# Optimization experiments

Hardware: AMD Instinct MI355X
Metric: run time of the kernel (lower is better)

## Reference

```python
import jax, jax.numpy as jnp
import numpy as np

N_ATOMS = 8192
N_PAIRS = 65536
F = 128        # n_atombasis
R = 20         # n_radialbasis
B = 5          # graph_n_blocks
EPS = 1e-8     # stability constant


def setup_inputs() -> dict:
    key = jax.random.key(0)
    ks = jax.random.split(key, 16)
    rn = lambda k, shape, s=0.05: jax.random.normal(k, shape, dtype=jnp.float32) * s
    return {
        "features": jax.random.normal(ks[0], (N_ATOMS, F), jnp.float32),
        "distances": jax.random.uniform(ks[1], (N_PAIRS,), jnp.float32, 0.5, 5.0),
        "vectors": jax.random.normal(ks[2], (N_PAIRS, 3), jnp.float32),
        "cutoffs": jax.random.uniform(ks[3], (N_PAIRS,), jnp.float32),
        "rbfs": jax.random.normal(ks[4], (N_PAIRS, R), jnp.float32),
        "filter_W": rn(ks[5], (R, B * 3 * F)),
        "filter_b": jnp.zeros((B * 3 * F,), jnp.float32),
        "int_W1": rn(ks[6], (B, F, F)),
        "int_b1": jnp.zeros((B, F), jnp.float32),
        "int_W2": rn(ks[7], (B, F, 3 * F)),
        "int_b2": jnp.zeros((B, 3 * F), jnp.float32),
        "mix_Wv": rn(ks[8], (B, F, 2 * F)),
        "mix_W1": rn(ks[9], (B, 2 * F, F)),
        "mix_b1": jnp.zeros((B, F), jnp.float32),
        "mix_W2": rn(ks[10], (B, F, 3 * F)),
        "mix_b2": jnp.zeros((B, 3 * F), jnp.float32),
        "idx_i": jax.random.randint(ks[11], (N_PAIRS,), 0, N_ATOMS),
        "idx_j": jax.random.randint(ks[12], (N_PAIRS,), 0, N_ATOMS),
    }


def reference(features, distances, vectors, cutoffs, rbfs,
              filter_W, filter_b, int_W1, int_b1, int_W2, int_b2,
              mix_Wv, mix_W1, mix_b1, mix_W2, mix_b2, idx_i, idx_j):
    n_atoms = features.shape[0]
    # Cutoff-weighted radial filters, one (3F) chunk per block: [P, B*3F]
    descriptors = (rbfs @ filter_W + filter_b) * cutoffs[:, None]
    dir_ij = vectors / distances[:, None]                       # [P, 3]

    q = features[:, None, :]                                    # [N, 1, F]
    mu = jnp.zeros((n_atoms, 3, F), dtype=features.dtype)       # [N, 3, F]

    for b in range(B):
        # --- interaction block ---
        x = jax.nn.silu(q @ int_W1[b] + int_b1[b]) @ int_W2[b] + int_b2[b]  # [N,1,3F]
        Wij = descriptors[:, None, b * 3 * F:(b + 1) * 3 * F]               # [P,1,3F]
        xj = x[idx_j] * Wij                                                 # [P,1,3F]
        muj = mu[idx_j]                                                     # [P,3,F]
        dq, dmuR, dmumu = jnp.split(xj, 3, axis=-1)                         # [P,1,F] each
        dmu = dmuR * dir_ij[:, :, None] + dmumu * muj                       # [P,3,F]
        q = q + jax.ops.segment_sum(dq, idx_i, num_segments=n_atoms)
        mu = mu + jax.ops.segment_sum(dmu, idx_i, num_segments=n_atoms)

        # --- mixing block ---
        mu_V, mu_W = jnp.split(mu @ mix_Wv[b], 2, axis=-1)                  # [N,3,F] each
        mu_Vn = jnp.sqrt(jnp.sum(mu_V ** 2, axis=-2, keepdims=True) + EPS)  # [N,1,F]
        ctx = jnp.concatenate([q, mu_Vn], axis=-1)                          # [N,1,2F]
        y = jax.nn.silu(ctx @ mix_W1[b] + mix_b1[b]) @ mix_W2[b] + mix_b2[b]
        dq_i, dmu_i, dqmu_i = jnp.split(y, 3, axis=-1)                      # [N,1,F] each
        q = q + dq_i + dqmu_i * jnp.sum(mu_V * mu_W, axis=1, keepdims=True)
        mu = mu + dmu_i * mu_W

    return q[:, 0, :], mu
```

## Files before the change

### kernel.cpp

```cpp
#include <hip/hip_runtime.h>
#include <hip/hip_bf16.h>

#define NA 8192
#define NP 65536
#define WROW 1920
#define CAP 40
#define PLANE 1048576

typedef short short8 __attribute__((ext_vector_type(8)));
typedef short short4v __attribute__((ext_vector_type(4)));
typedef float floatx4 __attribute__((ext_vector_type(4)));

static __device__ __forceinline__ short f2bf(float f) {
    union { float f; unsigned u; } v; v.f = f;
    unsigned r = v.u + 0x7FFF + ((v.u >> 16) & 1);
    return (short)(r >> 16);
}
static __device__ __forceinline__ float bf2f(short s) {
    union { unsigned u; float f; } v;
    v.u = ((unsigned)(unsigned short)s) << 16;
    return v.f;
}
static __device__ __forceinline__ unsigned char f2fp8(float f) {
    int p = __builtin_amdgcn_cvt_pk_fp8_f32(f, 0.f, 0, false);
    return (unsigned char)(p & 0xFF);
}
static __device__ __forceinline__ float fp82f(unsigned char b) {
    return __builtin_amdgcn_cvt_f32_fp8((int)b, 0);
}
static __device__ __forceinline__ float silu(float v) {
    return v / (1.f + __expf(-v));
}

static __device__ __forceinline__ void swz(const float* __restrict__ src,
                                           short* __restrict__ dst,
                                           int K, int N, int idx) {
    int kn = K * N;
    int b = idx / kn;
    int r = idx - b * kn;
    int tile = r >> 9, li = r & 511;
    int lane = li >> 3, bb = li & 7;
    int Kt = K >> 5;
    int nt = tile / Kt, kt = tile - nt * Kt;
    int k = kt * 32 + (lane >> 4) * 8 + bb;
    int n = nt * 16 + (lane & 15);
    dst[idx] = f2bf(src[b * kn + k * N + n]);
}

__global__ __launch_bounds__(256) void k_setup(const float* __restrict__ iW1,
                                               const float* __restrict__ iW2,
                                               const float* __restrict__ mWv,
                                               const float* __restrict__ mW1,
                                               const float* __restrict__ mW2,
                                               const float* __restrict__ fW,
                                               short* __restrict__ W1t,
                                               short* __restrict__ W2t,
                                               short* __restrict__ Wvt,
                                               short* __restrict__ mW1t,
                                               short* __restrict__ mW2t,
                                               short* __restrict__ fWt,
                                               const float* __restrict__ feat,
                                               float* __restrict__ q,
                                               float* __restrict__ mu,
                                               short* __restrict__ q_bf,
                                               unsigned short* __restrict__ mp0,
                                               int* __restrict__ cursor) {
    int idx = blockIdx.x * 256 + threadIdx.x;
    if (idx < 962560) {
        if (idx < 81920)       { swz(iW1, W1t, 128, 128, idx); return; }
        idx -= 81920;
        if (idx < 245760)      { swz(iW2, W2t, 128, 384, idx); return; }
        idx -= 245760;
        if (idx < 163840)      { swz(mWv, Wvt, 128, 256, idx); return; }
        idx -= 163840;
        if (idx < 163840)      { swz(mW1, mW1t, 256, 128, idx); return; }
        idx -= 163840;
        if (idx < 245760)      { swz(mW2, mW2t, 128, 384, idx); return; }
        idx -= 245760;
        {
            int b = idx / 12288;
            int r = idx - b * 12288;
            int nt = r >> 9;
            int li = r & 511;
            int lane = li >> 3, bb = li & 7;
            int k = (lane >> 4) * 8 + bb;
            int n = nt * 16 + (lane & 15);
            fWt[b * 12288 + r] = (k < 20) ? f2bf(fW[k * WROW + b * 384 + n]) : (short)0;
        }
        return;
    }
    idx -= 962560;
    if (idx < NA * 128) { float v = feat[idx]; q[idx] = v; q_bf[idx] = f2bf(v); }
    mu[idx] = 0.f;
    mp0[idx] = 0;
    if (idx < NA) cursor[idx] = 0;
}

__global__ __launch_bounds__(256) void k_fillprep(const int* __restrict__ idx_i,
                                                  const int* __restrict__ idx_j,
                                                  int* __restrict__ cursor,
                                                  const float* __restrict__ cut,
                                                  const float* __restrict__ dist,
                                                  const float* __restrict__ vec,
                                                  const float* __restrict__ rbfs,
                                                  float* __restrict__ cut_csr,
                                                  float4* __restrict__ dirj,
                                                  short* __restrict__ rbf_c) {
    int p = blockIdx.x * 256 + threadIdx.x;
    if (p >= NP) return;
    int i = idx_i[p];
    int pos = atomicAdd(&cursor[i], 1);
    if (pos >= CAP) return;
    int e = i * CAP + pos;
    float c = cut[p];
    cut_csr[e] = c;
    float invd = 1.f / dist[p];
    float4 d;
    d.x = vec[p * 3 + 0] * invd;
    d.y = vec[p * 3 + 1] * invd;
    d.z = vec[p * 3 + 2] * invd;
    d.w = __int_as_float(idx_j[p]);
    dirj[e] = d;
    #pragma unroll
    for (int k = 0; k < 20; ++k) rbf_c[e * 32 + k] = f2bf(rbfs[p * 20 + k] * c);
    #pragma unroll
    for (int k = 20; k < 32; ++k) rbf_c[e * 32 + k] = 0;
}

__global__ __launch_bounds__(256) void k_x(const short* __restrict__ q_bf,
                                           const short* __restrict__ W1sw,
                                           const short* __restrict__ W2sw,
                                           const float* __restrict__ b1,
                                           const float* __restrict__ b2,
                                           unsigned char* __restrict__ xp) {
    __shared__ __align__(16) short qtile[16 * 136];
    __shared__ __align__(16) short hs[16 * 136];
    int t = threadIdx.x;
    int wv = t >> 6, lane = t & 63, quad = lane >> 4, l16 = lane & 15;
    int a0 = blockIdx.x * 16;

    #pragma unroll
    for (int it = 0; it < 2; ++it) {
        int c = it * 256 + t;
        int row = c >> 5, col4 = c & 31;
        *(short4v*)(qtile + row * 136 + col4 * 4) =
            *(const short4v*)(q_bf + (a0 + row) * 128 + col4 * 4);
    }
    __syncthreads();

    floatx4 acc0 = {0.f, 0.f, 0.f, 0.f}, acc1 = {0.f, 0.f, 0.f, 0.f};
    #pragma unroll
    for (int kk = 0; kk < 4; ++kk) {
        short8 a  = *(const short8*)(qtile + l16 * 136 + kk * 32 + quad * 8);
        short8 b0 = *(const short8*)(W1sw + ((wv * 2 + 0) * 4 + kk) * 512 + lane * 8);
        short8 bq = *(const short8*)(W1sw + ((wv * 2 + 1) * 4 + kk) * 512 + lane * 8);
        acc0 = __builtin_amdgcn_mfma_f32_16x16x32_bf16(a, b0, acc0, 0, 0, 0);
        acc1 = __builtin_amdgcn_mfma_f32_16x16x32_bf16(a, bq, acc1, 0, 0, 0);
    }
    __syncthreads();
    {
        int n0 = wv * 32 + l16;
        float bia0 = b1[n0], bia1 = b1[n0 + 16];
        #pragma unroll
        for (int r = 0; r < 4; ++r) {
            int m = quad * 4 + r;
            hs[m * 136 + n0]      = f2bf(silu(acc0[r] + bia0));
            hs[m * 136 + n0 + 16] = f2bf(silu(acc1[r] + bia1));
        }
    }
    __syncthreads();
    floatx4 acc[6];
    #pragma unroll
    for (int jj = 0; jj < 6; ++jj) acc[jj] = {0.f, 0.f, 0.f, 0.f};
    #pragma unroll
    for (int kk = 0; kk < 4; ++kk) {
        short8 a = *(const short8*)(hs + l16 * 136 + kk * 32 + quad * 8);
        #pragma unroll
        for (int jj = 0; jj < 6; ++jj) {
            short8 b = *(const short8*)(W2sw + ((wv * 6 + jj) * 4 + kk) * 512 + lane * 8);
            acc[jj] = __builtin_amdgcn_mfma_f32_16x16x32_bf16(a, b, acc[jj], 0, 0, 0);
        }
    }
    #pragma unroll
    for (int jj = 0; jj < 6; ++jj) {
        int n = wv * 96 + jj * 16 + l16;
        float bia = b2[n];
        #pragma unroll
        for (int r = 0; r < 4; ++r) {
            int m = quad * 4 + r;
            xp[(size_t)(n >> 7) * PLANE + (size_t)(a0 + m) * 128 + (n & 127)] =
                f2fp8(acc[jj][r] + bia);
        }
    }
}

__global__ __launch_bounds__(256, 4) void k_gather(const unsigned char* __restrict__ xp_r,
                                                   const unsigned short* __restrict__ mp_r,
                                                   const short* __restrict__ rbf_c,
                                                   const short* __restrict__ fWt,
                                                   const float* __restrict__ fbp,
                                                   const float4* __restrict__ dirj,
                                                   const float* __restrict__ cut_csr,
                                                   const int* __restrict__ cursor,
                                                   short* __restrict__ dqg,
                                                   short* __restrict__ dmug) {
    __shared__ short dlds[16 * 392];
    __shared__ float pm[3 * 512];
    int i = blockIdx.x;
    int t = threadIdx.x;
    int wv = t >> 6, lane = t & 63, quad = lane >> 4, l16 = lane & 15;
    int start = i * CAP;
    int f0 = lane * 2;

    float4 dj[4];
    #pragma unroll
    for (int m = 0; m < 4; ++m) dj[m] = dirj[start + wv + 4 * m];
    short8 afrag = *(const short8*)(rbf_c + (size_t)(start + l16) * 32 + quad * 8);
    float cc[4];
    #pragma unroll
    for (int r = 0; r < 4; ++r) cc[r] = cut_csr[start + quad * 4 + r];

    int cnt = cursor[i];
    if (cnt > CAP) cnt = CAP;
    int end = start + cnt;

    float acc[8];
    #pragma unroll
    for (int k = 0; k < 8; ++k) acc[k] = 0.f;

    for (int e0 = start; e0 < end; e0 += 16) {
        if (e0 > start) {
            __syncthreads();
            #pragma unroll
            for (int m = 0; m < 4; ++m) dj[m] = dirj[e0 + wv + 4 * m];
            afrag = *(const short8*)(rbf_c + (size_t)(e0 + l16) * 32 + quad * 8);
            #pragma unroll
            for (int r = 0; r < 4; ++r) cc[r] = cut_csr[e0 + quad * 4 + r];
        }
        int clen = end - e0; if (clen > 16) clen = 16;
        #pragma unroll
        for (int nt = 0; nt < 6; ++nt) {
            int col = wv * 96 + nt * 16 + l16;
            short8 bfr = *(const short8*)(fWt + (wv * 6 + nt) * 512 + lane * 8);
            floatx4 z = {0.f, 0.f, 0.f, 0.f};
            floatx4 ad = __builtin_amdgcn_mfma_f32_16x16x32_bf16(afrag, bfr, z, 0, 0, 0);
            float fbv = fbp[col];
            dlds[(quad * 4 + 0) * 392 + col] = f2bf(ad[0] + fbv * cc[0]);
            dlds[(quad * 4 + 1) * 392 + col] = f2bf(ad[1] + fbv * cc[1]);
            dlds[(quad * 4 + 2) * 392 + col] = f2bf(ad[2] + fbv * cc[2]);
            dlds[(quad * 4 + 3) * 392 + col] = f2bf(ad[3] + fbv * cc[3]);
        }
        unsigned short xr0[4], xr1[4], xr2[4];
        unsigned mr0[4], mr1[4], mr2[4];
        #pragma unroll
        for (int m = 0; m < 4; ++m) {
            int le = wv + 4 * m;
            int j = (le < clen) ? __float_as_int(dj[m].w) : 0;
            size_t bx = (size_t)j * 128 + f0;
            xr0[m] = *(const unsigned short*)(xp_r + bx);
            xr1[m] = *(const unsigned short*)(xp_r + PLANE + bx);
            xr2[m] = *(const unsigned short*)(xp_r + 2 * PLANE + bx);
            mr0[m] = *(const unsigned*)(mp_r + bx);
            mr1[m] = *(const unsigned*)(mp_r + PLANE + bx);
            mr2[m] = *(const unsigned*)(mp_r + 2 * PLANE + bx);
        }
        __syncthreads();
        #pragma unroll
        for (int m = 0; m < 4; ++m) {
            int le = wv + 4 * m;
            if (le < clen) {
                unsigned wa = *(const unsigned*)(dlds + le * 392 + f0);
                unsigned wb = *(const unsigned*)(dlds + le * 392 + 128 + f0);
                unsigned wc = *(const unsigned*)(dlds + le * 392 + 256 + f0);
                float wa0 = bf2f((short)(wa & 0xFFFF)), wa1 = bf2f((short)(wa >> 16));
                float wb0 = bf2f((short)(wb & 0xFFFF)), wb1 = bf2f((short)(wb >> 16));
                float wc0 = bf2f((short)(wc & 0xFFFF)), wc1 = bf2f((short)(wc >> 16));
                {
                    float x0 = fp82f((unsigned char)(xr0[m] & 0xFF));
                    float x1 = fp82f((unsigned char)(xr1[m] & 0xFF));
                    float x2 = fp82f((unsigned char)(xr2[m] & 0xFF));
                    float u0 = bf2f((short)(mr0[m] & 0xFFFF));
                    float u1 = bf2f((short)(mr1[m] & 0xFFFF));
                    float u2 = bf2f((short)(mr2[m] & 0xFFFF));
                    acc[0] += x0 * wa0;
                    float xb = x1 * wb0, xc = x2 * wc0;
                    acc[1] += xb * dj[m].x + xc * u0;
                    acc[2] += xb * dj[m].y + xc * u1;
                    acc[3] += xb * dj[m].z + xc * u2;
                }
                {
                    float x0 = fp82f((unsigned char)(xr0[m] >> 8));
                    float x1 = fp82f((unsigned char)(xr1[m] >> 8));
                    float x2 = fp82f((unsigned char)(xr2[m] >> 8));
                    float u0 = bf2f((short)(mr0[m] >> 16));
                    float u1 = bf2f((short)(mr1[m] >> 16));
                    float u2 = bf2f((short)(mr2[m] >> 16));
                    acc[4] += x0 * wa1;
                    float xb = x1 * wb1, xc = x2 * wc1;
                    acc[5] += xb * dj[m].x + xc * u0;
                    acc[6] += xb * dj[m].y + xc * u1;
                    acc[7] += xb * dj[m].z + xc * u2;
                }
            }
        }
    }
    if (wv) {
        float* p = pm + (wv - 1) * 512;
        #pragma unroll
        for (int arr = 0; arr < 4; ++arr) {
            float2 v; v.x = acc[arr]; v.y = acc[arr + 4];
            *(float2*)(p + arr * 128 + f0) = v;
        }
    }
    __syncthreads();
    if (wv == 0) {
        #pragma unroll
        for (int arr = 0; arr < 4; ++arr) {
            float2 p0 = *(const float2*)(pm + 0 * 512 + arr * 128 + f0);
            float2 p1 = *(const float2*)(pm + 1 * 512 + arr * 128 + f0);
            float2 p2 = *(const float2*)(pm + 2 * 512 + arr * 128 + f0);
            float sl = acc[arr]     + p0.x + p1.x + p2.x;
            float sh = acc[arr + 4] + p0.y + p1.y + p2.y;
            unsigned o = (unsigned)(unsigned short)f2bf(sl) |
                         ((unsigned)(unsigned short)f2bf(sh) << 16);
            if (arr == 0) *(unsigned*)(dqg + i * 128 + f0) = o;
            else          *(unsigned*)(dmug + (i * 3 + arr - 1) * 128 + f0) = o;
        }
    }
}

__global__ __launch_bounds__(512, 4) void k_mixx(const float* __restrict__ mu_ro,
                                                 const short* __restrict__ dmug,
                                                 const float* __restrict__ q_ro,
                                                 const short* __restrict__ dqg,
                                                 const short* __restrict__ Wvsw,
                                                 const short* __restrict__ W1sw,
                                                 const short* __restrict__ W2sw,
                                                 const float* __restrict__ b1,
                                                 const float* __restrict__ b2,
                                                 float* __restrict__ q,
                                                 float* __restrict__ mu,
                                                 unsigned char* __restrict__ xp_w,
                                                 unsigned short* __restrict__ mp_w,
                                                 const short* __restrict__ xW1sw,
                                                 const short* __restrict__ xW2sw,
                                                 const float* __restrict__ xb1,
                                                 const float* __restrict__ xb2,
                                                 int do_x) {
    __shared__ __align__(16) char smem[51968];
    short* ms    = (short*)(smem);
    short* qtile = (short*)(smem + 13056);
    short* Vv    = (short*)(smem + 17408);
    short* hs    = (short*)(smem + 17408);
    short* Vw    = (short*)(smem + 30464);
    short* vnb   = (short*)(smem + 43520);
    short* sb    = (short*)(smem + 47872);
    unsigned char* xls = (unsigned char*)(smem + 43520);
    int t = threadIdx.x;
    int wv = t >> 6, lane = t & 63, quad = lane >> 4, l16 = lane & 15;
    int a0 = blockIdx.x * 16;
    int co = wv * 16 + l16;

    float qnf[4];
    float mnf[4][3];
    #pragma unroll
    for (int r = 0; r < 4; ++r) {
        int m = quad * 4 + r;
        int ga = a0 + m;
        int gq = ga * 128 + co;
        qnf[r] = q_ro[gq] + bf2f(dqg[gq]);
        qtile[m * 136 + co] = f2bf(qnf[r]);
        #pragma unroll
        for (int d = 0; d < 3; ++d) {
            int gm = (ga * 3 + d) * 128 + co;
            mnf[r][d] = mu_ro[gm] + bf2f(dmug[gm]);
            ms[(m * 3 + d) * 136 + co] = f2bf(mnf[r][d]);
        }
    }
    __syncthreads();

    {
        floatx4 acc[3][2];
        #pragma unroll
        for (int mt = 0; mt < 3; ++mt)
            #pragma unroll
            for (int nt = 0; nt < 2; ++nt) acc[mt][nt] = {0.f, 0.f, 0.f, 0.f};
        #pragma unroll
        for (int kk = 0; kk < 4; ++kk) {
            short8 a[3];
            #pragma unroll
            for (int mt = 0; mt < 3; ++mt)
                a[mt] = *(const short8*)(ms + (mt * 16 + l16) * 136 + kk * 32 + quad * 8);
            #pragma unroll
            for (int nt = 0; nt < 2; ++nt) {
                short8 b = *(const short8*)(Wvsw + ((wv * 2 + nt) * 4 + kk) * 512 + lane * 8);
                #pragma unroll
                for (int mt = 0; mt < 3; ++mt)
                    acc[mt][nt] = __builtin_amdgcn_mfma_f32_16x16x32_bf16(a[mt], b, acc[mt][nt], 0, 0, 0);
            }
        }
        #pragma unroll
        for (int mt = 0; mt < 3; ++mt)
            #pragma unroll
            for (int nt = 0; nt < 2; ++nt)
                #pragma unroll
                for (int r = 0; r < 4; ++r) {
                    int row = mt * 16 + quad * 4 + r;
                    int col = wv * 32 + nt * 16 + l16;
                    short v = f2bf(acc[mt][nt][r]);
                    if (col < 128) Vv[row * 136 + col] = v;
                    else           Vw[row * 136 + col - 128] = v;
                }
    }
    __syncthreads();
    #pragma unroll
    for (int k = 0; k < 4; ++k) {
        int idx = k * 512 + t;
        int a = idx >> 7, c = idx & 127;
        float v0 = bf2f(Vv[(a * 3 + 0) * 136 + c]);
        float v1 = bf2f(Vv[(a * 3 + 1) * 136 + c]);
        float v2 = bf2f(Vv[(a * 3 + 2) * 136 + c]);
        float w0 = bf2f(Vw[(a * 3 + 0) * 136 + c]);
        float w1 = bf2f(Vw[(a * 3 + 1) * 136 + c]);
        float w2 = bf2f(Vw[(a * 3 + 2) * 136 + c]);
        vnb[a * 136 + c] = f2bf(sqrtf(v0 * v0 + v1 * v1 + v2 * v2 + 1e-8f));
        sb[a * 128 + c]  = f2bf(v0 * w0 + v1 * w1 + v2 * w2);
    }
    __syncthreads();
    {
        floatx4 accq = {0.f, 0.f, 0.f, 0.f};
        floatx4 accv = {0.f, 0.f, 0.f, 0.f};
        #pragma unroll
        for (int kk = 0; kk < 4; ++kk) {
            short8 aq = *(const short8*)(qtile + l16 * 136 + kk * 32 + quad * 8);
            short8 av = *(const short8*)(vnb + l16 * 136 + kk * 32 + quad * 8);
            short8 bq = *(const short8*)(W1sw + (wv * 8 + kk) * 512 + lane * 8);
            short8 bv = *(const short8*)(W1sw + (wv * 8 + 4 + kk) * 512 + lane * 8);
            accq = __builtin_amdgcn_mfma_f32_16x16x32_bf16(aq, bq, accq, 0, 0, 0);
            accv = __builtin_amdgcn_mfma_f32_16x16x32_bf16(av, bv, accv, 0, 0, 0);
        }
        int n0 = wv * 16 + l16;
        float bia0 = b1[n0];
        #pragma unroll
        for (int r = 0; r < 4; ++r) {
            int m = quad * 4 + r;
            hs[m * 136 + n0] = f2bf(silu(accq[r] + accv[r] + bia0));
        }
    }
    __syncthreads();
    {
        floatx4 accB[3];
        #pragma unroll
        for (int c = 0; c < 3; ++c) accB[c] = {0.f, 0.f, 0.f, 0.f};
        #pragma unroll
        for (int kk = 0; kk < 4; ++kk) {
            short8 a = *(const short8*)(hs + l16 * 136 + kk * 32 + quad * 8);
            #pragma unroll
            for (int c = 0; c < 3; ++c) {
                short8 b = *(const short8*)(W2sw + ((c * 8 + wv) * 4 + kk) * 512 + lane * 8);
                accB[c] = __builtin_amdgcn_mfma_f32_16x16x32_bf16(a, b, accB[c], 0, 0, 0);
            }
        }
        float bq_  = b2[co];
        float bm_  = b2[128 + co];
        float bqm_ = b2[256 + co];
        #pragma unroll
        for (int r = 0; r < 4; ++r) {
            int m = quad * 4 + r;
            int ga = a0 + m;
            float dq   = accB[0][r] + bq_;
            float dmu  = accB[1][r] + bm_;
            float dqmu = accB[2][r] + bqm_;
            float sv = bf2f(sb[m * 128 + co]);
            int gq = ga * 128 + co;
            float qn = qnf[r] + dq + dqmu * sv;
            q[gq] = qn;
            qtile[m * 136 + co] = f2bf(qn);
            float mn[3];
            #pragma unroll
            for (int d = 0; d < 3; ++d) {
                int gm = (ga * 3 + d) * 128 + co;
                float mw = bf2f(Vw[(m * 3 + d) * 136 + co]);
                mn[d] = mnf[r][d] + dmu * mw;
                mu[gm] = mn[d];
            }
            if (do_x) {
                mp_w[(size_t)0 * PLANE + gq] = (unsigned short)f2bf(mn[0]);
                mp_w[(size_t)1 * PLANE + gq] = (unsigned short)f2bf(mn[1]);
                mp_w[(size_t)2 * PLANE + gq] = (unsigned short)f2bf(mn[2]);
            }
        }
    }
    if (!do_x) return;
    __syncthreads();
    {
        floatx4 acc0 = {0.f, 0.f, 0.f, 0.f};
        #pragma unroll
        for (int kk = 0; kk < 4; ++kk) {
            short8 a  = *(const short8*)(qtile + l16 * 136 + kk * 32 + quad * 8);
            short8 b0 = *(const short8*)(xW1sw + (wv * 4 + kk) * 512 + lane * 8);
            acc0 = __builtin_amdgcn_mfma_f32_16x16x32_bf16(a, b0, acc0, 0, 0, 0);
        }
        int n0 = wv * 16 + l16;
        float bia0 = xb1[n0];
        #pragma unroll
        for (int r = 0; r < 4; ++r) {
            int m = quad * 4 + r;
            hs[m * 136 + n0] = f2bf(silu(acc0[r] + bia0));
        }
    }
    __syncthreads();
    {
        floatx4 acc[3];
        #pragma unroll
        for (int jj = 0; jj < 3; ++jj) acc[jj] = {0.f, 0.f, 0.f, 0.f};
        #pragma unroll
        for (int kk = 0; kk < 4; ++kk) {
            short8 a = *(const short8*)(hs + l16 * 136 + kk * 32 + quad * 8);
            #pragma unroll
            for (int jj = 0; jj < 3; ++jj) {
                short8 b = *(const short8*)(xW2sw + ((wv * 3 + jj) * 4 + kk) * 512 + lane * 8);
                acc[jj] = __builtin_amdgcn_mfma_f32_16x16x32_bf16(a, b, acc[jj], 0, 0, 0);
            }
        }
        #pragma unroll
        for (int jj = 0; jj < 3; ++jj) {
            int n = wv * 48 + jj * 16 + l16;
            float bia = xb2[n];
            #pragma unroll
            for (int r = 0; r < 4; ++r) {
                int m = quad * 4 + r;
                xls[(n >> 7) * 2048 + m * 128 + (n & 127)] = f2fp8(acc[jj][r] + bia);
            }
        }
    }
    __syncthreads();
    {
        const unsigned* xlsu = (const unsigned*)xls;
        #pragma unroll
        for (int k = 0; k < 3; ++k) {
            int idx = k * 512 + t;
            int p = idx >> 9;
            int wo = idx & 511;
            *(unsigned*)(xp_w + (size_t)p * PLANE + (size_t)a0 * 128 + wo * 4) = xlsu[idx];
        }
    }
}

extern "C" void kernel_launch(void* const* d_in, const int* in_sizes, int n_in,
                              void* d_out, int out_size, void* d_ws, size_t ws_size,
                              hipStream_t stream) {
    const float* feat = (const float*)d_in[0];
    const float* dist = (const float*)d_in[1];
    const float* vec  = (const float*)d_in[2];
    const float* cut  = (const float*)d_in[3];
    const float* rbfs = (const float*)d_in[4];
    const float* fW   = (const float*)d_in[5];
    const float* fb   = (const float*)d_in[6];
    const float* iW1  = (const float*)d_in[7];
    const float* ib1  = (const float*)d_in[8];
    const float* iW2  = (const float*)d_in[9];
    const float* ib2  = (const float*)d_in[10];
    const float* mWv  = (const float*)d_in[11];
    const float* mW1  = (const float*)d_in[12];
    const float* mb1  = (const float*)d_in[13];
    const float* mW2  = (const float*)d_in[14];
    const float* mb2  = (const float*)d_in[15];
    const int* idx_i  = (const int*)d_in[16];
    const int* idx_j  = (const int*)d_in[17];

    float* q  = (float*)d_out;
    float* mu = (float*)d_out + NA * 128;

    char* w = (char*)d_ws;
    unsigned char*  xp0 = (unsigned char*)(w);
    unsigned char*  xp1 = (unsigned char*)(w + 3145728);
    unsigned short* mp0 = (unsigned short*)(w + 6291456);
    unsigned short* mp1 = (unsigned short*)(w + 12582912);
    short* dqg     = (short*)(w + 18874368);
    short* dmug    = (short*)(w + 20971520);
    short* q_bf    = (short*)(w + 27262976);
    short* W1t     = (short*)(w + 29360128);
    short* W2t     = (short*)(w + 29523968);
    short* Wvt     = (short*)(w + 30015488);
    short* mW1t    = (short*)(w + 30343168);
    short* mW2t    = (short*)(w + 30670848);
    short* fWt     = (short*)(w + 31162368);
    int*   cursor  = (int*)(w + 31285248);
    float4* dirj   = (float4*)(w + 31318016);
    float* cut_csr = (float*)(w + 36561152);
    short* rbf_c   = (short*)(w + 37871936);

    k_setup<<<16048, 256, 0, stream>>>(iW1, iW2, mWv, mW1, mW2, fW,
                                       W1t, W2t, Wvt, mW1t, mW2t, fWt,
                                       feat, q, mu, q_bf, mp0, cursor);
    k_fillprep<<<NP / 256, 256, 0, stream>>>(idx_i, idx_j, cursor, cut, dist, vec,
                                             rbfs, cut_csr, dirj, rbf_c);

    k_x<<<NA / 16, 256, 0, stream>>>(q_bf, W1t, W2t, ib1, ib2, xp0);
    unsigned char*  xa[2] = {xp0, xp1};
    unsigned short* ma[2] = {mp0, mp1};
    for (int b = 0; b < 5; ++b) {
        int bn = (b + 1) % 5;
        k_gather<<<NA, 256, 0, stream>>>(xa[b & 1], ma[b & 1], rbf_c, fWt + b * 12288,
                                         fb + b * 384, dirj, cut_csr, cursor,
                                         dqg, dmug);
        k_mixx<<<NA / 16, 512, 0, stream>>>(mu, dmug, q, dqg,
                                            Wvt + b * 32768,
                                            mW1t + b * 32768, mW2t + b * 49152,
                                            mb1 + b * 128, mb2 + b * 384,
                                            q, mu,
                                            xa[(b + 1) & 1], ma[(b + 1) & 1],
                                            W1t + bn * 16384, W2t + bn * 49152,
                                            ib1 + bn * 128, ib2 + bn * 384,
                                            (b < 4) ? 1 : 0);
    }
}
```

Measured before the change: 356.3 us.

## Process four atoms per gather block with prefetch of next atom's edge data

Each k_gather block now handles four consecutive atoms instead of one, so the grid shrinks by a factor of four. The per-edge direction, rbf fragment and cutoff values for the next atom are loaded during the last chunk of the current atom so their latency overlaps compute. This cuts block launch and setup overhead, but each block runs serially over its atoms with extra barriers and uses more registers. That can reduce occupancy and leave fewer blocks to hide gather latency.

```diff
diff --git a/kernel.cpp b/kernel.cpp
--- a/kernel.cpp
+++ b/kernel.cpp
@@ -206,125 +206,159 @@
                                                    short* __restrict__ dmug) {
     __shared__ short dlds[16 * 392];
     __shared__ float pm[3 * 512];
-    int i = blockIdx.x;
     int t = threadIdx.x;
     int wv = t >> 6, lane = t & 63, quad = lane >> 4, l16 = lane & 15;
-    int start = i * CAP;
     int f0 = lane * 2;
-
-    float4 dj[4];
-    #pragma unroll
-    for (int m = 0; m < 4; ++m) dj[m] = dirj[start + wv + 4 * m];
-    short8 afrag = *(const short8*)(rbf_c + (size_t)(start + l16) * 32 + quad * 8);
-    float cc[4];
-    #pragma unroll
-    for (int r = 0; r < 4; ++r) cc[r] = cut_csr[start + quad * 4 + r];
-
-    int cnt = cursor[i];
-    if (cnt > CAP) cnt = CAP;
-    int end = start + cnt;
-
-    float acc[8];
-    #pragma unroll
-    for (int k = 0; k < 8; ++k) acc[k] = 0.f;
-
-    for (int e0 = start; e0 < end; e0 += 16) {
-        if (e0 > start) {
+    int base = blockIdx.x * 4;
+    int4 cnt4 = *(const int4*)(cursor + base);
+
+    float4 dj[4]; short8 afrag; float cc[4];
+    {
+        int s0 = base * CAP;
+        #pragma unroll
+        for (int m = 0; m < 4; ++m) dj[m] = dirj[s0 + wv + 4 * m];
+        afrag = *(const short8*)(rbf_c + (size_t)(s0 + l16) * 32 + quad * 8);
+        #pragma unroll
+        for (int r = 0; r < 4; ++r) cc[r] = cut_csr[s0 + quad * 4 + r];
+    }
+    float4 djP[4]; short8 afP; float ccP[4]; int pfv = 0;
+
+    for (int ai = 0; ai < 4; ++ai) {
+        int i = base + ai;
+        int start = i * CAP;
+        int cnt = (ai == 0) ? cnt4.x : (ai == 1) ? cnt4.y : (ai == 2) ? cnt4.z : cnt4.w;
+        if (cnt > CAP) cnt = CAP;
+        int end = start + cnt;
+
+        if (ai > 0) {
+            if (pfv) {
+                #pragma unroll
+                for (int m = 0; m < 4; ++m) dj[m] = djP[m];
+                afrag = afP;
+                #pragma unroll
+                for (int r = 0; r < 4; ++r) cc[r] = ccP[r];
+            } else {
+                #pragma unroll
+                for (int m = 0; m < 4; ++m) dj[m] = dirj[start + wv + 4 * m];
+                afrag = *(const short8*)(rbf_c + (size_t)(start + l16) * 32 + quad * 8);
+                #pragma unroll
+                for (int r = 0; r < 4; ++r) cc[r] = cut_csr[start + quad * 4 + r];
+            }
+            pfv = 0;
+        }
+
+        float acc[8];
+        #pragma unroll
+        for (int k = 0; k < 8; ++k) acc[k] = 0.f;
+
+        for (int e0 = start; e0 < end; e0 += 16) {
+            if (e0 > start) {
+                __syncthreads();
+                #pragma unroll
+                for (int m = 0; m < 4; ++m) dj[m] = dirj[e0 + wv + 4 * m];
+                afrag = *(const short8*)(rbf_c + (size_t)(e0 + l16) * 32 + quad * 8);
+                #pragma unroll
+                for (int r = 0; r < 4; ++r) cc[r] = cut_csr[e0 + quad * 4 + r];
+            }
+            int clen = end - e0; if (clen > 16) clen = 16;
+            #pragma unroll
+            for (int nt = 0; nt < 6; ++nt) {
+                int col = wv * 96 + nt * 16 + l16;
+                short8 bfr = *(const short8*)(fWt + (wv * 6 + nt) * 512 + lane * 8);
+                floatx4 z = {0.f, 0.f, 0.f, 0.f};
+                floatx4 ad = __builtin_amdgcn_mfma_f32_16x16x32_bf16(afrag, bfr, z, 0, 0, 0);
+                float fbv = fbp[col];
+                dlds[(quad * 4 + 0) * 392 + col] = f2bf(ad[0] + fbv * cc[0]);
+                dlds[(quad * 4 + 1) * 392 + col] = f2bf(ad[1] + fbv * cc[1]);
+                dlds[(quad * 4 + 2) * 392 + col] = f2bf(ad[2] + fbv * cc[2]);
+                dlds[(quad * 4 + 3) * 392 + col] = f2bf(ad[3] + fbv * cc[3]);
+            }
+            unsigned short xr0[4], xr1[4], xr2[4];
+            unsigned mr0[4], mr1[4], mr2[4];
+            #pragma unroll
+            for (int m = 0; m < 4; ++m) {
+                int le = wv + 4 * m;
+                int j = (le < clen) ? __float_as_int(dj[m].w) : 0;
+                size_t bx = (size_t)j * 128 + f0;
+                xr0[m] = *(const unsigned short*)(xp_r + bx);
+                xr1[m] = *(const unsigned short*)(xp_r + PLANE + bx);
+                xr2[m] = *(const unsigned short*)(xp_r + 2 * PLANE + bx);
+                mr0[m] = *(const unsigned*)(mp_r + bx);
+                mr1[m] = *(const unsigned*)(mp_r + PLANE + bx);
+                mr2[m] = *(const unsigned*)(mp_r + 2 * PLANE + bx);
+            }
+            if (ai < 3 && e0 + 16 >= end && !pfv) {
+                int s2 = (i + 1) * CAP;
+                #pragma unroll
+                for (int m = 0; m < 4; ++m) djP[m] = dirj[s2 + wv + 4 * m];
+                afP = *(const short8*)(rbf_c + (size_t)(s2 + l16) * 32 + quad * 8);
+                #pragma unroll
+                for (int r = 0; r < 4; ++r) ccP[r] = cut_csr[s2 + quad * 4 + r];
+                pfv = 1;
+            }
             __syncthreads();
             #pragma unroll
-            for (int m = 0; m < 4; ++m) dj[m] = dirj[e0 + wv + 4 * m];
-            afrag = *(const short8*)(rbf_c + (size_t)(e0 + l16) * 32 + quad * 8);
-            #pragma unroll
-            for (int r = 0; r < 4; ++r) cc[r] = cut_csr[e0 + quad * 4 + r];
-        }
-        int clen = end - e0; if (clen > 16) clen = 16;
-        #pragma unroll
-        for (int nt = 0; nt < 6; ++nt) {
-            int col = wv * 96 + nt * 16 + l16;
-            short8 bfr = *(const short8*)(fWt + (wv * 6 + nt) * 512 + lane * 8);
-            floatx4 z = {0.f, 0.f, 0.f, 0.f};
-            floatx4 ad = __builtin_amdgcn_mfma_f32_16x16x32_bf16(afrag, bfr, z, 0, 0, 0);
-            float fbv = fbp[col];
-            dlds[(quad * 4 + 0) * 392 + col] = f2bf(ad[0] + fbv * cc[0]);
-            dlds[(quad * 4 + 1) * 392 + col] = f2bf(ad[1] + fbv * cc[1]);
-            dlds[(quad * 4 + 2) * 392 + col] = f2bf(ad[2] + fbv * cc[2]);
-            dlds[(quad * 4 + 3) * 392 + col] = f2bf(ad[3] + fbv * cc[3]);
-        }
-        unsigned short xr0[4], xr1[4], xr2[4];
-        unsigned mr0[4], mr1[4], mr2[4];
-        #pragma unroll
-        for (int m = 0; m < 4; ++m) {
-            int le = wv + 4 * m;
-            int j = (le < clen) ? __float_as_int(dj[m].w) : 0;
-            size_t bx = (size_t)j * 128 + f0;
-            xr0[m] = *(const unsigned short*)(xp_r + bx);
-            xr1[m] = *(const unsigned short*)(xp_r + PLANE + bx);
-            xr2[m] = *(const unsigned short*)(xp_r + 2 * PLANE + bx);
-            mr0[m] = *(const unsigned*)(mp_r + bx);
-            mr1[m] = *(const unsigned*)(mp_r + PLANE + bx);
-            mr2[m] = *(const unsigned*)(mp_r + 2 * PLANE + bx);
+            for (int m = 0; m < 4; ++m) {
+                int le = wv + 4 * m;
+                if (le < clen) {
+                    unsigned wa = *(const unsigned*)(dlds + le * 392 + f0);
+                    unsigned wb = *(const unsigned*)(dlds + le * 392 + 128 + f0);
+                    unsigned wc = *(const unsigned*)(dlds + le * 392 + 256 + f0);
+                    float wa0 = bf2f((short)(wa & 0xFFFF)), wa1 = bf2f((short)(wa >> 16));
+                    float wb0 = bf2f((short)(wb & 0xFFFF)), wb1 = bf2f((short)(wb >> 16));
+                    float wc0 = bf2f((short)(wc & 0xFFFF)), wc1 = bf2f((short)(wc >> 16));
+                    {
+                        float x0 = fp82f((unsigned char)(xr0[m] & 0xFF));
+                        float x1 = fp82f((unsigned char)(xr1[m] & 0xFF));
+                        float x2 = fp82f((unsigned char)(xr2[m] & 0xFF));
+                        float u0 = bf2f((short)(mr0[m] & 0xFFFF));
+                        float u1 = bf2f((short)(mr1[m] & 0xFFFF));
+                        float u2 = bf2f((short)(mr2[m] & 0xFFFF));
+                        acc[0] += x0 * wa0;
+                        float xb = x1 * wb0, xc = x2 * wc0;
+                        acc[1] += xb * dj[m].x + xc * u0;
+                        acc[2] += xb * dj[m].y + xc * u1;
+                        acc[3] += xb * dj[m].z + xc * u2;
+                    }
+                    {
+                        float x0 = fp82f((unsigned char)(xr0[m] >> 8));
+                        float x1 = fp82f((unsigned char)(xr1[m] >> 8));
+                        float x2 = fp82f((unsigned char)(xr2[m] >> 8));
+                        float u0 = bf2f((short)(mr0[m] >> 16));
+                        float u1 = bf2f((short)(mr1[m] >> 16));
+                        float u2 = bf2f((short)(mr2[m] >> 16));
+                        acc[4] += x0 * wa1;
+                        float xb = x1 * wb1, xc = x2 * wc1;
+                        acc[5] += xb * dj[m].x + xc * u0;
+                        acc[6] += xb * dj[m].y + xc * u1;
+                        acc[7] += xb * dj[m].z + xc * u2;
+                    }
+                }
+            }
         }
         __syncthreads();
-        #pragma unroll
-        for (int m = 0; m < 4; ++m) {
-            int le = wv + 4 * m;
-            if (le < clen) {
-                unsigned wa = *(const unsigned*)(dlds + le * 392 + f0);
-                unsigned wb = *(const unsigned*)(dlds + le * 392 + 128 + f0);
-                unsigned wc = *(const unsigned*)(dlds + le * 392 + 256 + f0);
-                float wa0 = bf2f((short)(wa & 0xFFFF)), wa1 = bf2f((short)(wa >> 16));
-                float wb0 = bf2f((short)(wb & 0xFFFF)), wb1 = bf2f((short)(wb >> 16));
-                float wc0 = bf2f((short)(wc & 0xFFFF)), wc1 = bf2f((short)(wc >> 16));
-                {
-                    float x0 = fp82f((unsigned char)(xr0[m] & 0xFF));
-                    float x1 = fp82f((unsigned char)(xr1[m] & 0xFF));
-                    float x2 = fp82f((unsigned char)(xr2[m] & 0xFF));
-                    float u0 = bf2f((short)(mr0[m] & 0xFFFF));
-                    float u1 = bf2f((short)(mr1[m] & 0xFFFF));
-                    float u2 = bf2f((short)(mr2[m] & 0xFFFF));
-                    acc[0] += x0 * wa0;
-                    float xb = x1 * wb0, xc = x2 * wc0;
-                    acc[1] += xb * dj[m].x + xc * u0;
-                    acc[2] += xb * dj[m].y + xc * u1;
-                    acc[3] += xb * dj[m].z + xc * u2;
-                }
-                {
-                    float x0 = fp82f((unsigned char)(xr0[m] >> 8));
-                    float x1 = fp82f((unsigned char)(xr1[m] >> 8));
-                    float x2 = fp82f((unsigned char)(xr2[m] >> 8));
-                    float u0 = bf2f((short)(mr0[m] >> 16));
-                    float u1 = bf2f((short)(mr1[m] >> 16));
-                    float u2 = bf2f((short)(mr2[m] >> 16));
-                    acc[4] += x0 * wa1;
-                    float xb = x1 * wb1, xc = x2 * wc1;
-                    acc[5] += xb * dj[m].x + xc * u0;
-                    acc[6] += xb * dj[m].y + xc * u1;
-                    acc[7] += xb * dj[m].z + xc * u2;
-                }
-            }
-        }
-    }
-    if (wv) {
-        float* p = pm + (wv - 1) * 512;
-        #pragma unroll
-        for (int arr = 0; arr < 4; ++arr) {
-            float2 v; v.x = acc[arr]; v.y = acc[arr + 4];
-            *(float2*)(p + arr * 128 + f0) = v;
-        }
-    }
-    __syncthreads();
-    if (wv == 0) {
-        #pragma unroll
-        for (int arr = 0; arr < 4; ++arr) {
-            float2 p0 = *(const float2*)(pm + 0 * 512 + arr * 128 + f0);
-            float2 p1 = *(const float2*)(pm + 1 * 512 + arr * 128 + f0);
-            float2 p2 = *(const float2*)(pm + 2 * 512 + arr * 128 + f0);
-            float sl = acc[arr]     + p0.x + p1.x + p2.x;
-            float sh = acc[arr + 4] + p0.y + p1.y + p2.y;
-            unsigned o = (unsigned)(unsigned short)f2bf(sl) |
-                         ((unsigned)(unsigned short)f2bf(sh) << 16);
-            if (arr == 0) *(unsigned*)(dqg + i * 128 + f0) = o;
-            else          *(unsigned*)(dmug + (i * 3 + arr - 1) * 128 + f0) = o;
+        if (wv) {
+            float* p = pm + (wv - 1) * 512;
+            #pragma unroll
+            for (int arr = 0; arr < 4; ++arr) {
+                float2 v; v.x = acc[arr]; v.y = acc[arr + 4];
+                *(float2*)(p + arr * 128 + f0) = v;
+            }
+        }
+        __syncthreads();
+        if (wv == 0) {
+            #pragma unroll
+            for (int arr = 0; arr < 4; ++arr) {
+                float2 p0 = *(const float2*)(pm + 0 * 512 + arr * 128 + f0);
+                float2 p1 = *(const float2*)(pm + 1 * 512 + arr * 128 + f0);
+                float2 p2 = *(const float2*)(pm + 2 * 512 + arr * 128 + f0);
+                float sl = acc[arr]     + p0.x + p1.x + p2.x;
+                float sh = acc[arr + 4] + p0.y + p1.y + p2.y;
+                unsigned o = (unsigned)(unsigned short)f2bf(sl) |
+                             ((unsigned)(unsigned short)f2bf(sh) << 16);
+                if (arr == 0) *(unsigned*)(dqg + i * 128 + f0) = o;
+                else          *(unsigned*)(dmug + (i * 3 + arr - 1) * 128 + f0) = o;
+            }
         }
     }
 }
@@ -602,9 +636,9 @@
     unsigned short* ma[2] = {mp0, mp1};
     for (int b = 0; b < 5; ++b) {
         int bn = (b + 1) % 5;
-        k_gather<<<NA, 256, 0, stream>>>(xa[b & 1], ma[b & 1], rbf_c, fWt + b * 12288,
-                                         fb + b * 384, dirj, cut_csr, cursor,
-                                         dqg, dmug);
+        k_gather<<<NA / 4, 256, 0, stream>>>(xa[b & 1], ma[b & 1], rbf_c, fWt + b * 12288,
+                                             fb + b * 384, dirj, cut_csr, cursor,
+                                             dqg, dmug);
         k_mixx<<<NA / 16, 512, 0, stream>>>(mu, dmug, q, dqg,
                                             Wvt + b * 32768,
                                             mW1t + b * 32768, mW2t + b * 49152,
```

Result: slower. 564.8 us (+58.5%).

## Assign one wavefront per atom in gather kernel, removing block syncs and reduction

Applied to the files above, without the earlier changes.

The gather kernel now maps each wavefront to its own destination atom (four atoms per block) rather than spreading one atom's edges across four waves. Each wave computes its own descriptor tile with 24 MFMAs over 8-edge chunks, keeps it in a private LDS slice, and accumulates directly, which removes the __syncthreads barriers and the cross-wave LDS reduction. The cost is that each wave does the full descriptor MFMA work, with half of the 16-row MFMA output discarded because only 8 edges are used per chunk, and the per-wave gather loads run more serially with less latency hiding.

```diff
diff --git a/kernel.cpp b/kernel.cpp
--- a/kernel.cpp
+++ b/kernel.cpp
@@ -204,22 +204,14 @@
                                                    const int* __restrict__ cursor,
                                                    short* __restrict__ dqg,
                                                    short* __restrict__ dmug) {
-    __shared__ short dlds[16 * 392];
-    __shared__ float pm[3 * 512];
-    int i = blockIdx.x;
+    __shared__ short dldsA[4][8 * 392];
     int t = threadIdx.x;
     int wv = t >> 6, lane = t & 63, quad = lane >> 4, l16 = lane & 15;
+    int f0 = lane * 2;
+    int i = blockIdx.x * 4 + wv;
+    short* dld = dldsA[wv];
+
     int start = i * CAP;
-    int f0 = lane * 2;
-
-    float4 dj[4];
-    #pragma unroll
-    for (int m = 0; m < 4; ++m) dj[m] = dirj[start + wv + 4 * m];
-    short8 afrag = *(const short8*)(rbf_c + (size_t)(start + l16) * 32 + quad * 8);
-    float cc[4];
-    #pragma unroll
-    for (int r = 0; r < 4; ++r) cc[r] = cut_csr[start + quad * 4 + r];
-
     int cnt = cursor[i];
     if (cnt > CAP) cnt = CAP;
     int end = start + cnt;
@@ -228,34 +220,20 @@
     #pragma unroll
     for (int k = 0; k < 8; ++k) acc[k] = 0.f;
 
-    for (int e0 = start; e0 < end; e0 += 16) {
-        if (e0 > start) {
-            __syncthreads();
-            #pragma unroll
-            for (int m = 0; m < 4; ++m) dj[m] = dirj[e0 + wv + 4 * m];
-            afrag = *(const short8*)(rbf_c + (size_t)(e0 + l16) * 32 + quad * 8);
-            #pragma unroll
-            for (int r = 0; r < 4; ++r) cc[r] = cut_csr[e0 + quad * 4 + r];
-        }
-        int clen = end - e0; if (clen > 16) clen = 16;
-        #pragma unroll
-        for (int nt = 0; nt < 6; ++nt) {
-            int col = wv * 96 + nt * 16 + l16;
-            short8 bfr = *(const short8*)(fWt + (wv * 6 + nt) * 512 + lane * 8);
-            floatx4 z = {0.f, 0.f, 0.f, 0.f};
-            floatx4 ad = __builtin_amdgcn_mfma_f32_16x16x32_bf16(afrag, bfr, z, 0, 0, 0);
-            float fbv = fbp[col];
-            dlds[(quad * 4 + 0) * 392 + col] = f2bf(ad[0] + fbv * cc[0]);
-            dlds[(quad * 4 + 1) * 392 + col] = f2bf(ad[1] + fbv * cc[1]);
-            dlds[(quad * 4 + 2) * 392 + col] = f2bf(ad[2] + fbv * cc[2]);
-            dlds[(quad * 4 + 3) * 392 + col] = f2bf(ad[3] + fbv * cc[3]);
-        }
+    for (int e0 = start; e0 < end; e0 += 8) {
+        int clen = end - e0; if (clen > 8) clen = 8;
+        float4 dj0[4];
+        #pragma unroll
+        for (int m = 0; m < 4; ++m) dj0[m] = dirj[e0 + m];
+        short8 afrag = *(const short8*)(rbf_c + (size_t)(e0 + l16) * 32 + quad * 8);
+        float cc[4];
+        #pragma unroll
+        for (int r = 0; r < 4; ++r) cc[r] = cut_csr[e0 + (quad & 1) * 4 + r];
         unsigned short xr0[4], xr1[4], xr2[4];
         unsigned mr0[4], mr1[4], mr2[4];
         #pragma unroll
         for (int m = 0; m < 4; ++m) {
-            int le = wv + 4 * m;
-            int j = (le < clen) ? __float_as_int(dj[m].w) : 0;
+            int j = (m < clen) ? __float_as_int(dj0[m].w) : 0;
             size_t bx = (size_t)j * 128 + f0;
             xr0[m] = *(const unsigned short*)(xp_r + bx);
             xr1[m] = *(const unsigned short*)(xp_r + PLANE + bx);
@@ -264,14 +242,25 @@
             mr1[m] = *(const unsigned*)(mp_r + PLANE + bx);
             mr2[m] = *(const unsigned*)(mp_r + 2 * PLANE + bx);
         }
-        __syncthreads();
+        #pragma unroll
+        for (int nt = 0; nt < 24; ++nt) {
+            short8 bfr = *(const short8*)(fWt + nt * 512 + lane * 8);
+            floatx4 z = {0.f, 0.f, 0.f, 0.f};
+            floatx4 ad = __builtin_amdgcn_mfma_f32_16x16x32_bf16(afrag, bfr, z, 0, 0, 0);
+            if (quad < 2) {
+                int col = nt * 16 + l16;
+                float fbv = fbp[col];
+                #pragma unroll
+                for (int r = 0; r < 4; ++r)
+                    dld[(quad * 4 + r) * 392 + col] = f2bf(ad[r] + fbv * cc[r]);
+            }
+        }
         #pragma unroll
         for (int m = 0; m < 4; ++m) {
-            int le = wv + 4 * m;
-            if (le < clen) {
-                unsigned wa = *(const unsigned*)(dlds + le * 392 + f0);
-                unsigned wb = *(const unsigned*)(dlds + le * 392 + 128 + f0);
-                unsigned wc = *(const unsigned*)(dlds + le * 392 + 256 + f0);
+            if (m < clen) {
+                unsigned wa = *(const unsigned*)(dld + m * 392 + f0);
+                unsigned wb = *(const unsigned*)(dld + m * 392 + 128 + f0);
+                unsigned wc = *(const unsigned*)(dld + m * 392 + 256 + f0);
                 float wa0 = bf2f((short)(wa & 0xFFFF)), wa1 = bf2f((short)(wa >> 16));
                 float wb0 = bf2f((short)(wb & 0xFFFF)), wb1 = bf2f((short)(wb >> 16));
                 float wc0 = bf2f((short)(wc & 0xFFFF)), wc1 = bf2f((short)(wc >> 16));
@@ -284,9 +273,9 @@
                     float u2 = bf2f((short)(mr2[m] & 0xFFFF));
                     acc[0] += x0 * wa0;
                     float xb = x1 * wb0, xc = x2 * wc0;
-                    acc[1] += xb * dj[m].x + xc * u0;
-                    acc[2] += xb * dj[m].y + xc * u1;
-                    acc[3] += xb * dj[m].z + xc * u2;
+                    acc[1] += xb * dj0[m].x + xc * u0;
+                    acc[2] += xb * dj0[m].y + xc * u1;
+                    acc[3] += xb * dj0[m].z + xc * u2;
                 }
                 {
                     float x0 = fp82f((unsigned char)(xr0[m] >> 8));
@@ -297,35 +286,73 @@
                     float u2 = bf2f((short)(mr2[m] >> 16));
                     acc[4] += x0 * wa1;
                     float xb = x1 * wb1, xc = x2 * wc1;
-                    acc[5] += xb * dj[m].x + xc * u0;
-                    acc[6] += xb * dj[m].y + xc * u1;
-                    acc[7] += xb * dj[m].z + xc * u2;
+                    acc[5] += xb * dj0[m].x + xc * u0;
+                    acc[6] += xb * dj0[m].y + xc * u1;
+                    acc[7] += xb * dj0[m].z + xc * u2;
                 }
             }
         }
-    }
-    if (wv) {
-        float* p = pm + (wv - 1) * 512;
-        #pragma unroll
-        for (int arr = 0; arr < 4; ++arr) {
-            float2 v; v.x = acc[arr]; v.y = acc[arr + 4];
-            *(float2*)(p + arr * 128 + f0) = v;
-        }
-    }
-    __syncthreads();
-    if (wv == 0) {
-        #pragma unroll
-        for (int arr = 0; arr < 4; ++arr) {
-            float2 p0 = *(const float2*)(pm + 0 * 512 + arr * 128 + f0);
-            float2 p1 = *(const float2*)(pm + 1 * 512 + arr * 128 + f0);
-            float2 p2 = *(const float2*)(pm + 2 * 512 + arr * 128 + f0);
-            float sl = acc[arr]     + p0.x + p1.x + p2.x;
-            float sh = acc[arr + 4] + p0.y + p1.y + p2.y;
-            unsigned o = (unsigned)(unsigned short)f2bf(sl) |
-                         ((unsigned)(unsigned short)f2bf(sh) << 16);
-            if (arr == 0) *(unsigned*)(dqg + i * 128 + f0) = o;
-            else          *(unsigned*)(dmug + (i * 3 + arr - 1) * 128 + f0) = o;
-        }
+        int c2 = clen - 4;
+        if (c2 > 0) {
+            #pragma unroll
+            for (int m = 0; m < 4; ++m) dj0[m] = dirj[e0 + 4 + m];
+            #pragma unroll
+            for (int m = 0; m < 4; ++m) {
+                int j = (m < c2) ? __float_as_int(dj0[m].w) : 0;
+                size_t bx = (size_t)j * 128 + f0;
+                xr0[m] = *(const unsigned short*)(xp_r + bx);
+                xr1[m] = *(const unsigned short*)(xp_r + PLANE + bx);
+                xr2[m] = *(const unsigned short*)(xp_r + 2 * PLANE + bx);
+                mr0[m] = *(const unsigned*)(mp_r + bx);
+                mr1[m] = *(const unsigned*)(mp_r + PLANE + bx);
+                mr2[m] = *(const unsigned*)(mp_r + 2 * PLANE + bx);
+            }
+            #pragma unroll
+            for (int m = 0; m < 4; ++m) {
+                if (m < c2) {
+                    int le = 4 + m;
+                    unsigned wa = *(const unsigned*)(dld + le * 392 + f0);
+                    unsigned wb = *(const unsigned*)(dld + le * 392 + 128 + f0);
+                    unsigned wc = *(const unsigned*)(dld + le * 392 + 256 + f0);
+                    float wa0 = bf2f((short)(wa & 0xFFFF)), wa1 = bf2f((short)(wa >> 16));
+                    float wb0 = bf2f((short)(wb & 0xFFFF)), wb1 = bf2f((short)(wb >> 16));
+                    float wc0 = bf2f((short)(wc & 0xFFFF)), wc1 = bf2f((short)(wc >> 16));
+                    {
+                        float x0 = fp82f((unsigned char)(xr0[m] & 0xFF));
+                        float x1 = fp82f((unsigned char)(xr1[m] & 0xFF));
+                        float x2 = fp82f((unsigned char)(xr2[m] & 0xFF));
+                        float u0 = bf2f((short)(mr0[m] & 0xFFFF));
+                        float u1 = bf2f((short)(mr1[m] & 0xFFFF));
+                        float u2 = bf2f((short)(mr2[m] & 0xFFFF));
+                        acc[0] += x0 * wa0;
+                        float xb = x1 * wb0, xc = x2 * wc0;
+                        acc[1] += xb * dj0[m].x + xc * u0;
+                        acc[2] += xb * dj0[m].y + xc * u1;
+                        acc[3] += xb * dj0[m].z + xc * u2;
+                    }
+                    {
+                        float x0 = fp82f((unsigned char)(xr0[m] >> 8));
+                        float x1 = fp82f((unsigned char)(xr1[m] >> 8));
+                        float x2 = fp82f((unsigned char)(xr2[m] >> 8));
+                        float u0 = bf2f((short)(mr0[m] >> 16));
+                        float u1 = bf2f((short)(mr1[m] >> 16));
+                        float u2 = bf2f((short)(mr2[m] >> 16));
+                        acc[4] += x0 * wa1;
+                        float xb = x1 * wb1, xc = x2 * wc1;
+                        acc[5] += xb * dj0[m].x + xc * u0;
+                        acc[6] += xb * dj0[m].y + xc * u1;
+                        acc[7] += xb * dj0[m].z + xc * u2;
+                    }
+                }
+            }
+        }
+    }
+    #pragma unroll
+    for (int arr = 0; arr < 4; ++arr) {
+        unsigned o = (unsigned)(unsigned short)f2bf(acc[arr]) |
+                     ((unsigned)(unsigned short)f2bf(acc[arr + 4]) << 16);
+        if (arr == 0) *(unsigned*)(dqg + i * 128 + f0) = o;
+        else          *(unsigned*)(dmug + (i * 3 + arr - 1) * 128 + f0) = o;
     }
 }
 
@@ -602,9 +629,9 @@
     unsigned short* ma[2] = {mp0, mp1};
     for (int b = 0; b < 5; ++b) {
         int bn = (b + 1) % 5;
-        k_gather<<<NA, 256, 0, stream>>>(xa[b & 1], ma[b & 1], rbf_c, fWt + b * 12288,
-                                         fb + b * 384, dirj, cut_csr, cursor,
-                                         dqg, dmug);
+        k_gather<<<NA / 4, 256, 0, stream>>>(xa[b & 1], ma[b & 1], rbf_c, fWt + b * 12288,
+                                             fb + b * 384, dirj, cut_csr, cursor,
+                                             dqg, dmug);
         k_mixx<<<NA / 16, 512, 0, stream>>>(mu, dmug, q, dqg,
                                             Wvt + b * 32768,
                                             mW1t + b * 32768, mW2t + b * 49152,
```

Result: slower. 622.8 us (+74.8%).
